# Kernel tuning notes

Measured on AMD Instinct MI355X. Metric: run time of the kernel, lower is better.

The kernel has to match this reference:

```python
import jax, jax.numpy as jnp
import numpy as np

N_NODES = 100000
N_EDGES = 1600000
IN_FEATS = 128
OUT_FEATS = 128
LN_EPS = 1e-5


def setup_inputs() -> dict:
    key = jax.random.key(0)
    k1, k2, k3, k4, k5 = jax.random.split(key, 5)
    h = jax.random.normal(k1, (N_NODES, IN_FEATS), dtype=jnp.float32)
    # nn.Linear(2*in_feats, out_feats): weight [out, 2*in], bias [out]
    stdv = 1.0 / np.sqrt(2 * IN_FEATS)
    W = jax.random.uniform(k2, (OUT_FEATS, 2 * IN_FEATS), dtype=jnp.float32, minval=-stdv, maxval=stdv)
    b = jax.random.uniform(k3, (OUT_FEATS,), dtype=jnp.float32, minval=-stdv, maxval=stdv)
    gamma = jnp.ones((OUT_FEATS,), dtype=jnp.float32)
    beta = jnp.zeros((OUT_FEATS,), dtype=jnp.float32)
    src = jax.random.randint(k4, (N_EDGES,), 0, N_NODES, dtype=jnp.int32)
    dst = jax.random.randint(k5, (N_EDGES,), 0, N_NODES, dtype=jnp.int32)
    return {"h": h, "W": W, "b": b, "gamma": gamma, "beta": beta, "src": src, "dst": dst}


def reference(h, W, b, gamma, beta, src, dst):
    n = h.shape[0]
    ones = jnp.ones(src.shape[0], dtype=h.dtype)
    deg = jax.ops.segment_sum(ones, dst, num_segments=n)          # in-degrees [N]
    norm = jnp.where(deg > 0, 1.0 / deg, 0.0)[:, None]            # inf -> 0
    ah = jax.ops.segment_sum(h[src], dst, num_segments=n)         # copy_src + sum: [N, D]
    cat = jnp.concatenate([h, ah * norm], axis=1)                 # [N, 2D]
    y = cat @ W.T + b                                             # linear -> [N, OUT]
    mu = jnp.mean(y, axis=-1, keepdims=True)
    var = jnp.mean((y - mu) ** 2, axis=-1, keepdims=True)
    y = (y - mu) * jax.lax.rsqrt(var + LN_EPS) * gamma + beta     # LayerNorm
    return jax.nn.relu(y)
```

## Files before the change

kernel.cpp:

```cpp
#include <hip/hip_runtime.h>
#include <hip/hip_bf16.h>

#define LN_EPS 1e-5f

#define NW 4096
#define CHUNK_CAP 96

#define CAP2 1280

#define S_MASK 0x1FFFFu

typedef __attribute__((ext_vector_type(8))) short short8;
typedef __attribute__((ext_vector_type(4))) float f32x4;
typedef __attribute__((ext_vector_type(2))) float f32x2;
typedef __attribute__((ext_vector_type(4))) int int4v;
typedef __attribute__((ext_vector_type(4))) unsigned int uint4v;

#if defined(__has_builtin)
# if __has_builtin(__builtin_amdgcn_cvt_pk_f32_fp8)
#  define HAS_HW_FP8 1
# endif
# if __has_builtin(__builtin_amdgcn_cvt_pk_fp8_f32)
#  define HAS_HW_FP8E 1
# endif
#endif
#ifndef HAS_HW_FP8
# define HAS_HW_FP8 0
#endif
#ifndef HAS_HW_FP8E
# define HAS_HW_FP8E 0
#endif

__device__ __forceinline__ float b2f(unsigned short u) {
    union { unsigned int i; float f; } x; x.i = ((unsigned int)u) << 16; return x.f;
}
__device__ __forceinline__ unsigned short f2b(float f) {
    unsigned int u = __float_as_uint(f);
    unsigned int r = (u + 0x7FFFu + ((u >> 16) & 1u)) >> 16;
    return (unsigned short)r;
}
__device__ __forceinline__ float loadf(const void* p, long long i, int flag) {
    return flag ? ((const float*)p)[i] : b2f(((const unsigned short*)p)[i]);
}

__device__ __forceinline__ unsigned char f2fp8(float x) {
    float ax = fabsf(x);
    unsigned char s = (unsigned char)((__float_as_uint(x) >> 24) & 0x80);
    if (ax >= 448.f) return s | 0x7E;
    if (ax < 0.015625f) {
        int m = (int)(ax * 512.f + 0.5f);
        return s | (unsigned char)m;
    }
    unsigned u = __float_as_uint(ax);
    int e = (int)((u >> 23) & 0xFF) - 127;
    unsigned m = u & 0x7FFFFF;
    unsigned mr = (m + 0x7FFFF + ((m >> 20) & 1)) >> 20;
    unsigned val = (unsigned)((e + 7) << 3) + mr;
    if (val > 0x7E) val = 0x7E;
    return s | (unsigned char)val;
}
__device__ __forceinline__ unsigned enc4(float a, float b, float c, float d) {
#if HAS_HW_FP8E
    int r = __builtin_amdgcn_cvt_pk_fp8_f32(a, b, 0, false);
    r = __builtin_amdgcn_cvt_pk_fp8_f32(c, d, r, true);
    return (unsigned)r;
#else
    return (unsigned)f2fp8(a) | ((unsigned)f2fp8(b) << 8) |
           ((unsigned)f2fp8(c) << 16) | ((unsigned)f2fp8(d) << 24);
#endif
}
__device__ __forceinline__ float fp8d(unsigned v) {
    unsigned s = (v & 0x80) << 24;
    unsigned e = (v >> 3) & 0xF;
    unsigned m = v & 7;
    if (e == 0) {
        float f = (float)m * 0.001953125f;
        return __uint_as_float(s | __float_as_uint(f));
    }
    return __uint_as_float(s | ((e + 120) << 23) | (m << 20));
}
__device__ __forceinline__ void dec16(uint4 u, float* acc) {
#if HAS_HW_FP8
    f32x2 p;
    p = __builtin_amdgcn_cvt_pk_f32_fp8((int)u.x, false); acc[0] += p[0];  acc[1] += p[1];
    p = __builtin_amdgcn_cvt_pk_f32_fp8((int)u.x, true);  acc[2] += p[0];  acc[3] += p[1];
    p = __builtin_amdgcn_cvt_pk_f32_fp8((int)u.y, false); acc[4] += p[0];  acc[5] += p[1];
    p = __builtin_amdgcn_cvt_pk_f32_fp8((int)u.y, true);  acc[6] += p[0];  acc[7] += p[1];
    p = __builtin_amdgcn_cvt_pk_f32_fp8((int)u.z, false); acc[8] += p[0];  acc[9] += p[1];
    p = __builtin_amdgcn_cvt_pk_f32_fp8((int)u.z, true);  acc[10] += p[0]; acc[11] += p[1];
    p = __builtin_amdgcn_cvt_pk_f32_fp8((int)u.w, false); acc[12] += p[0]; acc[13] += p[1];
    p = __builtin_amdgcn_cvt_pk_f32_fp8((int)u.w, true);  acc[14] += p[0]; acc[15] += p[1];
#else
    acc[0] += fp8d(u.x & 0xFF); acc[1] += fp8d((u.x >> 8) & 0xFF);
    acc[2] += fp8d((u.x >> 16) & 0xFF); acc[3] += fp8d(u.x >> 24);
    acc[4] += fp8d(u.y & 0xFF); acc[5] += fp8d((u.y >> 8) & 0xFF);
    acc[6] += fp8d((u.y >> 16) & 0xFF); acc[7] += fp8d(u.y >> 24);
    acc[8] += fp8d(u.z & 0xFF); acc[9] += fp8d((u.z >> 8) & 0xFF);
    acc[10] += fp8d((u.z >> 16) & 0xFF); acc[11] += fp8d(u.z >> 24);
    acc[12] += fp8d(u.w & 0xFF); acc[13] += fp8d((u.w >> 8) & 0xFF);
    acc[14] += fp8d((u.w >> 16) & 0xFF); acc[15] += fp8d(u.w >> 24);
#endif
}

__global__ __launch_bounds__(256) void prep_cvt_kernel(
    const void* __restrict__ h, unsigned char* __restrict__ h8,
    int* __restrict__ cnt, int* __restrict__ flag, int n_nodes, int n16) {
    __shared__ int sflag;
    const int tid = threadIdx.x;
    if (tid < 64) {
        const unsigned short* hb = (const unsigned short*)h;
        int bad = 0;
        unsigned short u = hb[2 * tid];        int e = (u >> 7) & 0xFF; bad += (e < 96 || e > 135);
        u = hb[2 * (tid + 64)];                e = (u >> 7) & 0xFF;     bad += (e < 96 || e > 135);
#pragma unroll
        for (int off = 1; off < 64; off <<= 1) bad += __shfl_xor(bad, off);
        if (tid == 0) sflag = (bad > 32) ? 1 : 0;
    }
    __syncthreads();
    const int f = sflag;
    const int idx = blockIdx.x * 256 + tid;
    if (idx < n_nodes) cnt[idx] = 0;
    if (idx == 0) *flag = f;
    if (idx < n16) {
        long long base = (long long)idx * 16;
        uint4 o;
        if (f == 0) {
            const unsigned short* hp = (const unsigned short*)h + base;
            short8 v0 = *(const short8*)hp;
            short8 v1 = *(const short8*)(hp + 8);
            o.x = enc4(b2f((unsigned short)v0[0]), b2f((unsigned short)v0[1]),
                       b2f((unsigned short)v0[2]), b2f((unsigned short)v0[3]));
            o.y = enc4(b2f((unsigned short)v0[4]), b2f((unsigned short)v0[5]),
                       b2f((unsigned short)v0[6]), b2f((unsigned short)v0[7]));
            o.z = enc4(b2f((unsigned short)v1[0]), b2f((unsigned short)v1[1]),
                       b2f((unsigned short)v1[2]), b2f((unsigned short)v1[3]));
            o.w = enc4(b2f((unsigned short)v1[4]), b2f((unsigned short)v1[5]),
                       b2f((unsigned short)v1[6]), b2f((unsigned short)v1[7]));
        } else {
            const float* hf = (const float*)h + base;
            f32x4 a = *(const f32x4*)hf;
            f32x4 b4 = *(const f32x4*)(hf + 4);
            f32x4 c4 = *(const f32x4*)(hf + 8);
            f32x4 d4 = *(const f32x4*)(hf + 12);
            o.x = enc4(a[0], a[1], a[2], a[3]);
            o.y = enc4(b4[0], b4[1], b4[2], b4[3]);
            o.z = enc4(c4[0], c4[1], c4[2], c4[3]);
            o.w = enc4(d4[0], d4[1], d4[2], d4[3]);
        }
        *(uint4*)(h8 + base) = o;
    }
}

__global__ __launch_bounds__(256) void bin_kernel(
    const int* __restrict__ src, const int* __restrict__ dst,
    unsigned* __restrict__ bins,
    int* __restrict__ wcnt,
    int n_edges, int part_nodes) {
    const int g = blockIdx.x * 4 + (threadIdx.x >> 6);
    const int lane = threadIdx.x & 63;
    const int epw = (n_edges + NW - 1) / NW;
    const int e0 = g * epw;
    const int e1 = min(e0 + epw, n_edges);
    const unsigned long long below = (1ull << lane) - 1ull;
    const int t4 = part_nodes * 4, t2 = part_nodes * 2;

    int cur0 = 0, cur1 = 0, cur2 = 0, cur3 = 0, cur4 = 0, cur5 = 0, cur6 = 0, cur7 = 0;

    for (int e = e0 + lane;; e += 64) {
        const bool valid = (e < e1);
        if (!__ballot(valid)) break;
        int d = 0, s = 0;
        if (valid) {
            d = __builtin_nontemporal_load(&dst[e]);
            s = __builtin_nontemporal_load(&src[e]);
        }
        int p = 0, dd = d;
        if (dd >= t4) { p += 4; dd -= t4; }
        if (dd >= t2) { p += 2; dd -= t2; }
        if (dd >= part_nodes) { p += 1; dd -= part_nodes; }

        int myoff = CHUNK_CAP;
#pragma unroll
        for (int pp = 0; pp < 8; ++pp) {
            const unsigned long long m = __ballot(valid && (p == pp));
            const int rank = __popcll(m & below);
            const int n = __popcll(m);
            int c = (pp == 0) ? cur0 : (pp == 1) ? cur1 : (pp == 2) ? cur2 :
                    (pp == 3) ? cur3 : (pp == 4) ? cur4 : (pp == 5) ? cur5 :
                    (pp == 6) ? cur6 : cur7;
            if (valid && (p == pp)) myoff = c + rank;
            c += n;
            if (pp == 0) cur0 = c; else if (pp == 1) cur1 = c;
            else if (pp == 2) cur2 = c; else if (pp == 3) cur3 = c;
            else if (pp == 4) cur4 = c; else if (pp == 5) cur5 = c;
            else if (pp == 6) cur6 = c; else cur7 = c;
        }
        if (valid && myoff < CHUNK_CAP) {
            const unsigned pr = ((unsigned)dd << 17) | (unsigned)s;
            bins[((long long)g * 8 + p) * CHUNK_CAP + myoff] = pr;
        }
    }
    int myc = cur0;
    myc = (lane == 1) ? cur1 : myc;  myc = (lane == 2) ? cur2 : myc;
    myc = (lane == 3) ? cur3 : myc;  myc = (lane == 4) ? cur4 : myc;
    myc = (lane == 5) ? cur5 : myc;  myc = (lane == 6) ? cur6 : myc;
    myc = (lane == 7) ? cur7 : myc;
    if (lane < 8) wcnt[g * 8 + lane] = min(myc, CHUNK_CAP);
}

__global__ __launch_bounds__(256) void regroup_kernel(
    const unsigned* __restrict__ bins, const int* __restrict__ wcnt,
    unsigned* __restrict__ bins2, int* __restrict__ gcur,
    int part_nodes) {
    __shared__ int bcnt[256], gbase_s[256], bcur_s[256];
    const int part = blockIdx.x & 7;
    const int rng  = blockIdx.x >> 3;
    const int wbase = rng * 64;
    const int tid = threadIdx.x;
    const int lo = part * part_nodes;
    const int fb_lo = lo >> 6;
    bcnt[tid] = 0;
    __syncthreads();
    const int wv = tid >> 6, lane = tid & 63;
    for (int c = wv; c < 64; c += 4) {
        const int w = wbase + c;
        const int n = wcnt[w * 8 + part];
        const unsigned* cb = bins + ((long long)w * 8 + part) * CHUNK_CAP;
        for (int i = lane; i < n; i += 64) {
            const int node = lo + (int)(cb[i] >> 17);
            atomicAdd(&bcnt[(node >> 6) - fb_lo], 1);
        }
    }
    __syncthreads();
    {
        const int c = bcnt[tid];
        gbase_s[tid] = (c > 0) ? atomicAdd(&gcur[fb_lo + tid], c) : 0;
        bcur_s[tid] = 0;
    }
    __syncthreads();
    for (int c = wv; c < 64; c += 4) {
        const int w = wbase + c;
        const int n = wcnt[w * 8 + part];
        const unsigned* cb = bins + ((long long)w * 8 + part) * CHUNK_CAP;
        for (int i = lane; i < n; i += 64) {
            const unsigned pr = cb[i];
            const int node = lo + (int)(pr >> 17);
            const int lb = (node >> 6) - fb_lo;
            const int r = atomicAdd(&bcur_s[lb], 1);
            const int pos = gbase_s[lb] + r;
            if (pos < CAP2)
                bins2[(long long)(fb_lo + lb) * CAP2 + pos] =
                    ((unsigned)(node & 63) << 17) | (pr & S_MASK);
        }
    }
}

__global__ __launch_bounds__(256) void gather_gemm_ln_kernel(
    const unsigned char* __restrict__ h8,
    const unsigned* __restrict__ bins2,
    const int* __restrict__ gcur,
    const void* __restrict__ h,
    const void* __restrict__ W,
    const void* __restrict__ bias,
    const void* __restrict__ gamma,
    const void* __restrict__ beta,
    void* __restrict__ out,
    const int* __restrict__ flagp,
    int n_nodes) {

    __shared__ __align__(16) unsigned short Atile[64 * 264];
    __shared__ __align__(16) char pool[CAP2 * 4];
    __shared__ int ncnt[64], noff[64], ncur[64];
    __shared__ unsigned char perm[64];
    __shared__ float2 mrs[64];

    int* slist = (int*)pool;
    float2* pS = (float2*)pool;

    const int flag = *flagp;
    const int tid = threadIdx.x;
    const int fb = blockIdx.x;
    const int nb0 = fb << 6;

    {
        const int seg = tid & 31;
        const int r0 = tid >> 5;
        if (seg < 16) {
            if (flag == 0) {
                const unsigned short* hb = (const unsigned short*)h;
#pragma unroll
                for (int j = 0; j < 8; ++j) {
                    int row = r0 + j * 8;
                    int node = nb0 + row;
                    if (node >= n_nodes) node = n_nodes - 1;
                    short8 val = __builtin_nontemporal_load(
                        (const short8*)(hb + (long long)node * 128 + seg * 8));
                    *(short8*)&Atile[row * 264 + seg * 8] = val;
                }
            } else {
                const float* hfp = (const float*)h;
#pragma unroll
                for (int j = 0; j < 8; ++j) {
                    int row = r0 + j * 8;
                    int node = nb0 + row;
                    if (node >= n_nodes) node = n_nodes - 1;
                    const float* p = hfp + (long long)node * 128 + seg * 8;
                    f32x4 a = __builtin_nontemporal_load((const f32x4*)p);
                    f32x4 b4 = __builtin_nontemporal_load(((const f32x4*)p) + 1);
                    short8 val;
                    val[0] = (short)f2b(a[0]);  val[1] = (short)f2b(a[1]);
                    val[2] = (short)f2b(a[2]);  val[3] = (short)f2b(a[3]);
                    val[4] = (short)f2b(b4[0]); val[5] = (short)f2b(b4[1]);
                    val[6] = (short)f2b(b4[2]); val[7] = (short)f2b(b4[3]);
                    *(short8*)&Atile[row * 264 + seg * 8] = val;
                }
            }
        }
    }

    if (tid < 64) ncnt[tid] = 0;
    __syncthreads();
    const int T = min(gcur[fb], CAP2);
    const unsigned* bb = bins2 + (long long)fb * CAP2;
    for (int i = tid; i < T; i += 256) {
        const int ld = (int)(bb[i] >> 17);
        atomicAdd(&ncnt[ld], 1);
    }
    __syncthreads();
    if (tid < 64) {
        const int mydeg = ncnt[tid];
        int o = 0, rk = 0;
#pragma unroll 1
        for (int j = 0; j < 64; ++j) {
            const int dj = ncnt[j];
            o += (j < tid) ? dj : 0;
            rk += (dj > mydeg) || (dj == mydeg && j < tid);
        }
        noff[tid] = o; ncur[tid] = 0;
        perm[rk] = (unsigned char)tid;
    }
    __syncthreads();
    for (int i = tid; i < T; i += 256) {
        const unsigned pr = bb[i];
        const int ld = (int)(pr >> 17);
        const int r = atomicAdd(&ncur[ld], 1);
        slist[noff[ld] + r] = (int)(pr & S_MASK);
    }
    __syncthreads();

    const int wv = tid >> 6, lane = tid & 63, g = lane >> 3, li = lane & 7;
#pragma unroll 1
    for (int pass = 0; pass < 2; ++pass) {
        const int rank = (pass * 8 + g) * 4 + wv;
        const int ld = perm[rank];
        const int node = nb0 + ld;
        const bool nvalid = (node < n_nodes);
        const int deg = nvalid ? ncnt[ld] : 0;
        const int ofs = noff[ld];
        int mn = deg, mx = deg;
        mn = min(mn, __shfl_xor(mn, 8));  mx = max(mx, __shfl_xor(mx, 8));
        mn = min(mn, __shfl_xor(mn, 16)); mx = max(mx, __shfl_xor(mx, 16));
        mn = min(mn, __shfl_xor(mn, 32)); mx = max(mx, __shfl_xor(mx, 32));

        float acc[16];
#pragma unroll
        for (int j = 0; j < 16; ++j) acc[j] = 0.f;

        int e = 0;
        for (; e + 3 < mn; e += 4) {
            const int s0 = slist[ofs + e];
            const int s1 = slist[ofs + e + 1];
            const int s2 = slist[ofs + e + 2];
            const int s3 = slist[ofs + e + 3];
            uint4 u0 = *(const uint4*)(h8 + (long long)s0 * 128 + li * 16);
            uint4 u1 = *(const uint4*)(h8 + (long long)s1 * 128 + li * 16);
            uint4 u2 = *(const uint4*)(h8 + (long long)s2 * 128 + li * 16);
            uint4 u3 = *(const uint4*)(h8 + (long long)s3 * 128 + li * 16);
            dec16(u0, acc);
            dec16(u1, acc);
            dec16(u2, acc);
            dec16(u3, acc);
        }
        for (; e < mx; ++e) {
            const bool v = (e < deg);
            const int s = slist[min(ofs + (v ? e : 0), CAP2 - 1)];
            uint4 u = *(const uint4*)(h8 + (long long)(v ? s : 0) * 128 + li * 16);
            if (!v) { u.x = 0u; u.y = 0u; u.z = 0u; u.w = 0u; }
            dec16(u, acc);
        }

        const float nrm = deg > 0 ? 1.f / (float)deg : 0.f;
        short8 a0, a1;
        a0[0] = (short)f2b(acc[0] * nrm);  a0[1] = (short)f2b(acc[1] * nrm);
        a0[2] = (short)f2b(acc[2] * nrm);  a0[3] = (short)f2b(acc[3] * nrm);
        a0[4] = (short)f2b(acc[4] * nrm);  a0[5] = (short)f2b(acc[5] * nrm);
        a0[6] = (short)f2b(acc[6] * nrm);  a0[7] = (short)f2b(acc[7] * nrm);
        a1[0] = (short)f2b(acc[8] * nrm);  a1[1] = (short)f2b(acc[9] * nrm);
        a1[2] = (short)f2b(acc[10] * nrm); a1[3] = (short)f2b(acc[11] * nrm);
        a1[4] = (short)f2b(acc[12] * nrm); a1[5] = (short)f2b(acc[13] * nrm);
        a1[6] = (short)f2b(acc[14] * nrm); a1[7] = (short)f2b(acc[15] * nrm);
        *(short8*)&Atile[ld * 264 + 128 + li * 16] = a0;
        *(short8*)&Atile[ld * 264 + 128 + li * 16 + 8] = a1;
    }
    __syncthreads();

    const int q = lane >> 4;
    const int c = lane & 15;

    short8 bfrag[8][2];
    if (flag == 0) {
        const unsigned short* Wb = (const unsigned short*)W;
#pragma unroll
        for (int ki = 0; ki < 8; ++ki)
#pragma unroll
            for (int t2 = 0; t2 < 2; ++t2)
                bfrag[ki][t2] = *(const short8*)&Wb[(wv * 32 + t2 * 16 + c) * 256 + ki * 32 + q * 8];
    } else {
        const float* Wf = (const float*)W;
#pragma unroll
        for (int ki = 0; ki < 8; ++ki)
#pragma unroll
            for (int t2 = 0; t2 < 2; ++t2) {
                const float* p = Wf + (wv * 32 + t2 * 16 + c) * 256 + ki * 32 + q * 8;
#pragma unroll
                for (int j = 0; j < 8; ++j) bfrag[ki][t2][j] = (short)f2b(p[j]);
            }
    }

    f32x4 acc2[4][2];
#pragma unroll
    for (int rc = 0; rc < 4; ++rc)
#pragma unroll
        for (int t2 = 0; t2 < 2; ++t2) acc2[rc][t2] = (f32x4){0.f, 0.f, 0.f, 0.f};

#pragma unroll
    for (int ki = 0; ki < 8; ++ki) {
        const int kk = ki * 32 + q * 8;
#pragma unroll
        for (int rc = 0; rc < 4; ++rc) {
            const short8 a = *(const short8*)&Atile[(rc * 16 + c) * 264 + kk];
            acc2[rc][0] = __builtin_amdgcn_mfma_f32_16x16x32_bf16(a, bfrag[ki][0], acc2[rc][0], 0, 0, 0);
            acc2[rc][1] = __builtin_amdgcn_mfma_f32_16x16x32_bf16(a, bfrag[ki][1], acc2[rc][1], 0, 0, 0);
        }
    }

    float bcol[2], gcol[2], ecol[2];
#pragma unroll
    for (int t2 = 0; t2 < 2; ++t2) {
        int col = wv * 32 + t2 * 16 + c;
        bcol[t2] = loadf(bias, col, flag);
        gcol[t2] = loadf(gamma, col, flag);
        ecol[t2] = loadf(beta, col, flag);
    }

#pragma unroll
    for (int rc = 0; rc < 4; ++rc)
#pragma unroll
        for (int r = 0; r < 4; ++r) {
            float v0 = acc2[rc][0][r] + bcol[0];
            float v1 = acc2[rc][1][r] + bcol[1];
            float s = v0 + v1;
            float ss = v0 * v0 + v1 * v1;
            s += __shfl_xor(s, 1);  ss += __shfl_xor(ss, 1);
            s += __shfl_xor(s, 2);  ss += __shfl_xor(ss, 2);
            s += __shfl_xor(s, 4);  ss += __shfl_xor(ss, 4);
            s += __shfl_xor(s, 8);  ss += __shfl_xor(ss, 8);
            if (c == 0) {
                int row = rc * 16 + q * 4 + r;
                pS[row * 5 + wv] = make_float2(s, ss);
            }
        }
    __syncthreads();

    if (tid < 64) {
        float s = 0.f, ss = 0.f;
#pragma unroll
        for (int j = 0; j < 4; ++j) {
            float2 p = pS[tid * 5 + j];
            s += p.x; ss += p.y;
        }
        float mean = s * (1.f / 128.f);
        float var = ss * (1.f / 128.f) - mean * mean;
        mrs[tid] = make_float2(mean, rsqrtf(var + LN_EPS));
    }
    __syncthreads();

    if (flag == 0) {
        unsigned short* ostage = Atile;
#pragma unroll
        for (int rc = 0; rc < 4; ++rc)
#pragma unroll
            for (int r = 0; r < 4; ++r) {
                int row = rc * 16 + q * 4 + r;
                float2 m = mrs[row];
#pragma unroll
                for (int t2 = 0; t2 < 2; ++t2) {
                    float o = (acc2[rc][t2][r] + bcol[t2] - m.x) * m.y * gcol[t2] + ecol[t2];
                    o = o > 0.f ? o : 0.f;
                    ostage[row * 128 + wv * 32 + t2 * 16 + c] = f2b(o);
                }
            }
        __syncthreads();
        const uint4v* sv = (const uint4v*)Atile;
#pragma unroll
        for (int rdx = 0; rdx < 4; ++rdx) {
            int u = rdx * 256 + tid;
            int row = u >> 4;
            int node = nb0 + row;
            if (node < n_nodes)
                __builtin_nontemporal_store(sv[u],
                    (uint4v*)((unsigned short*)out + (long long)node * 128 + (u & 15) * 8));
        }
    } else {
        float* ostage = (float*)Atile;
#pragma unroll
        for (int rc = 0; rc < 4; ++rc)
#pragma unroll
            for (int r = 0; r < 4; ++r) {
                int row = rc * 16 + q * 4 + r;
                float2 m = mrs[row];
#pragma unroll
                for (int t2 = 0; t2 < 2; ++t2) {
                    float o = (acc2[rc][t2][r] + bcol[t2] - m.x) * m.y * gcol[t2] + ecol[t2];
                    o = o > 0.f ? o : 0.f;
                    ostage[row * 128 + wv * 32 + t2 * 16 + c] = o;
                }
            }
        __syncthreads();
        const uint4v* sv = (const uint4v*)Atile;
#pragma unroll
        for (int rdx = 0; rdx < 8; ++rdx) {
            int u = rdx * 256 + tid;
            int row = u >> 5;
            int node = nb0 + row;
            if (node < n_nodes)
                __builtin_nontemporal_store(sv[u],
                    (uint4v*)((float*)out + (long long)node * 128 + (u & 31) * 4));
        }
    }
}

extern "C" void kernel_launch(void* const* d_in, const int* in_sizes, int n_in,
                              void* d_out, int out_size, void* d_ws, size_t ws_size,
                              hipStream_t stream) {
    const void* h     = d_in[0];
    const void* W     = d_in[1];
    const void* b     = d_in[2];
    const void* gamma = d_in[3];
    const void* beta  = d_in[4];
    const int* src = (const int*)d_in[5];
    const int* dst = (const int*)d_in[6];

    const int n_nodes = in_sizes[0] / 128;
    const int n_edges = in_sizes[5];
    const int part_nodes = (n_nodes + 7) / 8;
    const int nbuckets = (n_nodes + 63) >> 6;

    unsigned short* reg0 = (unsigned short*)d_ws;
    unsigned* bins2 = (unsigned*)(reg0 + (size_t)n_nodes * 128);
    int* gcur   = (int*)bins2 + (size_t)n_nodes * 64;
    int* flag   = gcur + n_nodes;
    unsigned char* h8 = (unsigned char*)(flag + 64);

    unsigned* bins = (unsigned*)reg0;
    int* wcnt = (int*)((char*)reg0 + (size_t)NW * 8 * CHUNK_CAP * 4);

    int n16 = n_nodes * 8;
    int pgrid = (max(n16, n_nodes) + 255) / 256;
    prep_cvt_kernel<<<pgrid, 256, 0, stream>>>(h, h8, gcur, flag, n_nodes, n16);

    bin_kernel<<<NW / 4, 256, 0, stream>>>(src, dst, bins, wcnt, n_edges, part_nodes);

    regroup_kernel<<<512, 256, 0, stream>>>(bins, wcnt, bins2, gcur, part_nodes);

    gather_gemm_ln_kernel<<<nbuckets, 256, 0, stream>>>(h8, bins2, gcur, h, W, b,
                                                        gamma, beta, d_out, flag, n_nodes);
}
```

Baseline: 238.3 us.

## Fuse edge binning and regroup into a single scatter kernel reading dst directly

Removes the intermediate per-wave partition binning pass and its bins buffer. Each block now handles one edge range and one node partition, reading dst twice (count pass, then scatter pass) and keeping only edges whose destination falls in its partition. This drops one kernel launch and the write and read of the intermediate bins, at the cost of every edge range being read by 8 blocks. Output stores also switch from nontemporal to regular stores.

New measurement: 262.0 us. +9.9%, slower.

```diff
diff --git a/kernel.cpp b/kernel.cpp
--- a/kernel.cpp
+++ b/kernel.cpp
@@ -2,9 +2,6 @@
 #include <hip/hip_bf16.h>
 
 #define LN_EPS 1e-5f
-
-#define NW 4096
-#define CHUNK_CAP 96
 
 #define CAP2 1280
 
@@ -151,106 +148,44 @@
     }
 }
 
-__global__ __launch_bounds__(256) void bin_kernel(
+__global__ __launch_bounds__(1024) void scatter_kernel(
     const int* __restrict__ src, const int* __restrict__ dst,
-    unsigned* __restrict__ bins,
-    int* __restrict__ wcnt,
-    int n_edges, int part_nodes) {
-    const int g = blockIdx.x * 4 + (threadIdx.x >> 6);
-    const int lane = threadIdx.x & 63;
-    const int epw = (n_edges + NW - 1) / NW;
-    const int e0 = g * epw;
-    const int e1 = min(e0 + epw, n_edges);
-    const unsigned long long below = (1ull << lane) - 1ull;
-    const int t4 = part_nodes * 4, t2 = part_nodes * 2;
-
-    int cur0 = 0, cur1 = 0, cur2 = 0, cur3 = 0, cur4 = 0, cur5 = 0, cur6 = 0, cur7 = 0;
-
-    for (int e = e0 + lane;; e += 64) {
-        const bool valid = (e < e1);
-        if (!__ballot(valid)) break;
-        int d = 0, s = 0;
-        if (valid) {
-            d = __builtin_nontemporal_load(&dst[e]);
-            s = __builtin_nontemporal_load(&src[e]);
-        }
-        int p = 0, dd = d;
-        if (dd >= t4) { p += 4; dd -= t4; }
-        if (dd >= t2) { p += 2; dd -= t2; }
-        if (dd >= part_nodes) { p += 1; dd -= part_nodes; }
-
-        int myoff = CHUNK_CAP;
-#pragma unroll
-        for (int pp = 0; pp < 8; ++pp) {
-            const unsigned long long m = __ballot(valid && (p == pp));
-            const int rank = __popcll(m & below);
-            const int n = __popcll(m);
-            int c = (pp == 0) ? cur0 : (pp == 1) ? cur1 : (pp == 2) ? cur2 :
-                    (pp == 3) ? cur3 : (pp == 4) ? cur4 : (pp == 5) ? cur5 :
-                    (pp == 6) ? cur6 : cur7;
-            if (valid && (p == pp)) myoff = c + rank;
-            c += n;
-            if (pp == 0) cur0 = c; else if (pp == 1) cur1 = c;
-            else if (pp == 2) cur2 = c; else if (pp == 3) cur3 = c;
-            else if (pp == 4) cur4 = c; else if (pp == 5) cur5 = c;
-            else if (pp == 6) cur6 = c; else cur7 = c;
-        }
-        if (valid && myoff < CHUNK_CAP) {
-            const unsigned pr = ((unsigned)dd << 17) | (unsigned)s;
-            bins[((long long)g * 8 + p) * CHUNK_CAP + myoff] = pr;
-        }
-    }
-    int myc = cur0;
-    myc = (lane == 1) ? cur1 : myc;  myc = (lane == 2) ? cur2 : myc;
-    myc = (lane == 3) ? cur3 : myc;  myc = (lane == 4) ? cur4 : myc;
-    myc = (lane == 5) ? cur5 : myc;  myc = (lane == 6) ? cur6 : myc;
-    myc = (lane == 7) ? cur7 : myc;
-    if (lane < 8) wcnt[g * 8 + lane] = min(myc, CHUNK_CAP);
-}
-
-__global__ __launch_bounds__(256) void regroup_kernel(
-    const unsigned* __restrict__ bins, const int* __restrict__ wcnt,
     unsigned* __restrict__ bins2, int* __restrict__ gcur,
-    int part_nodes) {
+    int n_edges, int part_nodes, int n_nodes) {
     __shared__ int bcnt[256], gbase_s[256], bcur_s[256];
     const int part = blockIdx.x & 7;
     const int rng  = blockIdx.x >> 3;
-    const int wbase = rng * 64;
     const int tid = threadIdx.x;
     const int lo = part * part_nodes;
+    const int hi = min(lo + part_nodes, n_nodes);
     const int fb_lo = lo >> 6;
-    bcnt[tid] = 0;
-    __syncthreads();
-    const int wv = tid >> 6, lane = tid & 63;
-    for (int c = wv; c < 64; c += 4) {
-        const int w = wbase + c;
-        const int n = wcnt[w * 8 + part];
-        const unsigned* cb = bins + ((long long)w * 8 + part) * CHUNK_CAP;
-        for (int i = lane; i < n; i += 64) {
-            const int node = lo + (int)(cb[i] >> 17);
-            atomicAdd(&bcnt[(node >> 6) - fb_lo], 1);
-        }
-    }
-    __syncthreads();
-    {
+    const int epr = (n_edges + 63) >> 6;
+    const int e0 = rng * epr;
+    const int e1 = min(e0 + epr, n_edges);
+
+    if (tid < 256) bcnt[tid] = 0;
+    __syncthreads();
+    for (int e = e0 + tid; e < e1; e += 1024) {
+        const int d = __builtin_nontemporal_load(&dst[e]);
+        if (d >= lo && d < hi) atomicAdd(&bcnt[(d >> 6) - fb_lo], 1);
+    }
+    __syncthreads();
+    if (tid < 256) {
         const int c = bcnt[tid];
         gbase_s[tid] = (c > 0) ? atomicAdd(&gcur[fb_lo + tid], c) : 0;
         bcur_s[tid] = 0;
     }
     __syncthreads();
-    for (int c = wv; c < 64; c += 4) {
-        const int w = wbase + c;
-        const int n = wcnt[w * 8 + part];
-        const unsigned* cb = bins + ((long long)w * 8 + part) * CHUNK_CAP;
-        for (int i = lane; i < n; i += 64) {
-            const unsigned pr = cb[i];
-            const int node = lo + (int)(pr >> 17);
-            const int lb = (node >> 6) - fb_lo;
+    for (int e = e0 + tid; e < e1; e += 1024) {
+        const int d = __builtin_nontemporal_load(&dst[e]);
+        if (d >= lo && d < hi) {
+            const int s = __builtin_nontemporal_load(&src[e]);
+            const int lb = (d >> 6) - fb_lo;
             const int r = atomicAdd(&bcur_s[lb], 1);
             const int pos = gbase_s[lb] + r;
             if (pos < CAP2)
                 bins2[(long long)(fb_lo + lb) * CAP2 + pos] =
-                    ((unsigned)(node & 63) << 17) | (pr & S_MASK);
+                    ((unsigned)(d & 63) << 17) | (unsigned)s;
         }
     }
 }
@@ -508,8 +443,7 @@
             int row = u >> 4;
             int node = nb0 + row;
             if (node < n_nodes)
-                __builtin_nontemporal_store(sv[u],
-                    (uint4v*)((unsigned short*)out + (long long)node * 128 + (u & 15) * 8));
+                *(uint4v*)((unsigned short*)out + (long long)node * 128 + (u & 15) * 8) = sv[u];
         }
     } else {
         float* ostage = (float*)Atile;
@@ -534,8 +468,7 @@
             int row = u >> 5;
             int node = nb0 + row;
             if (node < n_nodes)
-                __builtin_nontemporal_store(sv[u],
-                    (uint4v*)((float*)out + (long long)node * 128 + (u & 31) * 4));
+                *(uint4v*)((float*)out + (long long)node * 128 + (u & 31) * 4) = sv[u];
         }
     }
 }
@@ -562,16 +495,12 @@
     int* flag   = gcur + n_nodes;
     unsigned char* h8 = (unsigned char*)(flag + 64);
 
-    unsigned* bins = (unsigned*)reg0;
-    int* wcnt = (int*)((char*)reg0 + (size_t)NW * 8 * CHUNK_CAP * 4);
-
     int n16 = n_nodes * 8;
     int pgrid = (max(n16, n_nodes) + 255) / 256;
     prep_cvt_kernel<<<pgrid, 256, 0, stream>>>(h, h8, gcur, flag, n_nodes, n16);
 
-    bin_kernel<<<NW / 4, 256, 0, stream>>>(src, dst, bins, wcnt, n_edges, part_nodes);
-
-    regroup_kernel<<<512, 256, 0, stream>>>(bins, wcnt, bins2, gcur, part_nodes);
+    scatter_kernel<<<512, 1024, 0, stream>>>(src, dst, bins2, gcur,
+                                             n_edges, part_nodes, n_nodes);
 
     gather_gemm_ln_kernel<<<nbuckets, 256, 0, stream>>>(h8, bins2, gcur, h, W, b,
                                                         gamma, beta, d_out, flag, n_nodes);
```
